# Performance work log

Hardware: AMD Instinct MI355X
Metric: run time of the kernel (lower is better)

## Reference

```python
import jax, jax.numpy as jnp
import numpy as np
from jax import lax

# Module constraint: hidden_dim == state_dim == expand_dim (see broadcasting in original).
H = 128  # hidden_dim
N = 128  # state_dim
E = 128  # expand_dim = hidden_dim * expand_factor (expand_factor=1)
B, L = 4, 1024


def setup_inputs() -> dict:
    key = jax.random.key(0)
    ks = jax.random.split(key, 11)
    s = lambda fan: 1.0 / np.sqrt(fan)
    return {
        "u": jax.random.normal(ks[0], (B, L, H), jnp.float32),
        "W_in": jax.random.normal(ks[1], (H, 2 * E), jnp.float32) * s(H),
        "b_in": jax.random.normal(ks[2], (2 * E,), jnp.float32) * 0.01,
        "conv_w": jax.random.normal(ks[3], (E, 1, 3), jnp.float32) * s(3),
        "conv_b": jax.random.normal(ks[4], (E,), jnp.float32) * 0.01,
        "W_x": jax.random.normal(ks[5], (E, N + N + H), jnp.float32) * s(E),
        "b_x": jax.random.normal(ks[6], (N + N + H,), jnp.float32) * 0.01,
        "A_log": jax.random.normal(ks[7], (N,), jnp.float32),
        "D": jnp.ones((H,), jnp.float32),
        "W_out": jax.random.normal(ks[8], (E, H), jnp.float32) * s(E),
        "b_out": jax.random.normal(ks[9], (H,), jnp.float32) * 0.01,
    }


def reference(u, W_in, b_in, conv_w, conv_b, W_x, b_x, A_log, D, W_out, b_out):
    b, l, _ = u.shape
    xz = u @ W_in + b_in                       # [B,L,2E]
    x, z = jnp.split(xz, 2, axis=-1)           # [B,L,E] each
    # depthwise conv1d, kernel 3, padding 1 (groups == channels)
    xc = lax.conv_general_dilated(
        x.transpose(0, 2, 1), conv_w, window_strides=(1,), padding=[(1, 1)],
        feature_group_count=E, dimension_numbers=("NCH", "OIH", "NCH"))
    x = jax.nn.silu(xc.transpose(0, 2, 1) + conv_b)  # [B,L,E]
    ssm = x @ W_x + b_x                        # [B,L,2N+H]
    delta = jax.nn.softplus(ssm[..., :N])      # [B,L,N]
    Bm = ssm[..., N:2 * N]                     # [B,L,N]
    C = ssm[..., 2 * N:]                       # [B,L,H]
    A = -jnp.exp(A_log)                        # [N]

    def step(h, inp):
        d_t, B_t, C_t, x_t, u_t = inp          # [B,N],[B,N],[B,H],[B,E],[B,H]
        # A_discrete[b,t,i,j] = exp(delta[b,t,i] * A[j])  (outer broadcast, as in source)
        A_disc = jnp.exp(d_t[:, :, None] * A[None, None, :])       # [B,N,N]
        h = A_disc * h + (d_t * B_t)[:, :, None] * x_t[:, None, :]  # [B,N,E]
        y = (h * C_t[:, None, :]).sum(axis=1) + D * u_t             # [B,H]
        return h, y

    h0 = jnp.zeros((b, N, H), u.dtype)
    inputs = (delta.transpose(1, 0, 2), Bm.transpose(1, 0, 2),
              C.transpose(1, 0, 2), x.transpose(1, 0, 2), u.transpose(1, 0, 2))
    _, ys = lax.scan(step, h0, inputs)         # ys: [L,B,H]
    y = ys.transpose(1, 0, 2) * jax.nn.silu(z)  # [B,L,H] (E==H)
    return y @ W_out + b_out                   # dropout in eval mode: identity
```

## Files before the change

### kernel.cpp

```cpp
#include <hip/hip_runtime.h>
#include <hip/hip_bf16.h>

using bf16 = __hip_bfloat16;
typedef __attribute__((ext_vector_type(8))) short short8;
typedef __attribute__((ext_vector_type(4))) float f32x4;

#define BVAL 4
#define LVAL 1024
#define LOG2E 1.44269504f

#define PTS 68

#define OFF_BIN    0
#define OFF_CONVW  256
#define OFF_CONVB  640
#define OFF_BX     768
#define OFF_ALOG   1152
#define OFF_D      1280
#define OFF_BOUT   1408
#define CVT_SMALL  1536

#define R_UBF   524288
#define R_WTIN  (R_UBF + 32768)
#define R_WTX   (R_WTIN + 49152)
#define R_WTOUT (R_WTX + 16384)
#define R_TOT   (R_WTOUT + CVT_SMALL)

__device__ __forceinline__ int dtype_flag(const void* D) {
    return ((*(const unsigned int*)D) & 0xFFFFu) != 0u ? 1 : 0;
}
__device__ __forceinline__ float ldin(const void* p, size_t i, int f) {
    return f ? __bfloat162float(((const bf16*)p)[i]) : ((const float*)p)[i];
}
__device__ __forceinline__ short f2bf(float x) {
    union { bf16 h; short s; } u; u.h = __float2bfloat16(x); return u.s;
}

__global__ void k0_cvt(const void* __restrict__ u, const void* __restrict__ W_in,
                       const void* __restrict__ b_in, const void* __restrict__ conv_w,
                       const void* __restrict__ conv_b, const void* __restrict__ W_x,
                       const void* __restrict__ b_x, const void* __restrict__ A_log,
                       const void* __restrict__ D, const void* __restrict__ W_out,
                       const void* __restrict__ b_out,
                       float* __restrict__ cvt, bf16* __restrict__ ubf,
                       bf16* __restrict__ wtin, bf16* __restrict__ wtx,
                       bf16* __restrict__ wtout) {
    int idx = blockIdx.x * 256 + threadIdx.x;
    if (idx >= R_TOT) return;
    int f = dtype_flag(D);
    if (idx < R_UBF) {
        ubf[idx] = __float2bfloat16(ldin(u, idx, f));
    } else if (idx < R_WTIN) {
        int rel = idx - R_UBF; int n = rel >> 7, k = rel & 127;
        wtin[rel] = __float2bfloat16(ldin(W_in, (size_t)k * 256 + n, f));
    } else if (idx < R_WTX) {
        int rel = idx - R_WTIN; int n = rel >> 7, k = rel & 127;
        wtx[rel] = __float2bfloat16(ldin(W_x, (size_t)k * 384 + n, f));
    } else if (idx < R_WTOUT) {
        int rel = idx - R_WTX; int n = rel >> 7, k = rel & 127;
        wtout[rel] = __float2bfloat16(ldin(W_out, (size_t)k * 128 + n, f));
    } else {
        int rel = idx - R_WTOUT; const void* p; int loc;
        if      (rel < 256)  { p = b_in;   loc = rel; }
        else if (rel < 640)  { p = conv_w; loc = rel - 256; }
        else if (rel < 768)  { p = conv_b; loc = rel - 640; }
        else if (rel < 1152) { p = b_x;    loc = rel - 768; }
        else if (rel < 1280) { p = A_log;  loc = rel - 1152; }
        else if (rel < 1408) { p = D;      loc = rel - 1280; }
        else                 { p = b_out;  loc = rel - 1408; }
        cvt[rel] = ldin(p, loc, f);
    }
}

__global__ void k1_mfma(const bf16* __restrict__ ubf, const bf16* __restrict__ wtin,
                        const float* __restrict__ cvt,
                        float* __restrict__ x_pre, float* __restrict__ zs) {
    int blk = blockIdx.x, mb = blk >> 3, cb = blk & 7;
    int tid = threadIdx.x, w = tid >> 6, lane = tid & 63;
    int quad = lane >> 4, sub = lane & 15;
    int m0 = mb * 64 + w * 16, c = cb * 16;
    f32x4 accX = {0.f, 0.f, 0.f, 0.f}, accZ = {0.f, 0.f, 0.f, 0.f};
    #pragma unroll
    for (int ks = 0; ks < 4; ++ks) {
        int k0 = ks * 32 + quad * 8;
        short8 a  = *(const short8*)(ubf + (size_t)(m0 + sub) * 128 + k0);
        short8 bX = *(const short8*)(wtin + (size_t)(c + sub) * 128 + k0);
        short8 bZ = *(const short8*)(wtin + (size_t)(128 + c + sub) * 128 + k0);
        accX = __builtin_amdgcn_mfma_f32_16x16x32_bf16(a, bX, accX, 0, 0, 0);
        accZ = __builtin_amdgcn_mfma_f32_16x16x32_bf16(a, bZ, accZ, 0, 0, 0);
    }
    int o = c + sub;
    float bx_ = cvt[OFF_BIN + o], bz_ = cvt[OFF_BIN + 128 + o];
    #pragma unroll
    for (int r = 0; r < 4; ++r) {
        int m = m0 + quad * 4 + r;
        float x = accX[r] + bx_;
        float z = accZ[r] + bz_;
        x_pre[(size_t)m * 128 + o] = x;
        zs[(size_t)m * 128 + o] = z / (1.0f + __expf(-z));
    }
}

__global__ void k3_mfma(const float* __restrict__ x_pre, const bf16* __restrict__ wtx,
                        const float* __restrict__ cvt, float* __restrict__ xT,
                        float* __restrict__ dT, float* __restrict__ wT,
                        float* __restrict__ CcT) {
    __shared__ float swc[128 * 4];
    int blk = blockIdx.x, mb = blk >> 3, cb = blk & 7;
    int tid = threadIdx.x, w = tid >> 6, lane = tid & 63;
    int quad = lane >> 4, sub = lane & 15;
    if (tid < 128) {
        swc[tid * 4 + 0] = cvt[OFF_CONVW + tid * 3 + 0];
        swc[tid * 4 + 1] = cvt[OFF_CONVW + tid * 3 + 1];
        swc[tid * 4 + 2] = cvt[OFF_CONVW + tid * 3 + 2];
        swc[tid * 4 + 3] = cvt[OFF_CONVB + tid];
    }
    __syncthreads();
    int m0 = mb * 64 + w * 16, c = cb * 16;
    int row = m0 + sub;
    int l = row & (LVAL - 1);
    const float* xr = x_pre + (size_t)row * 128;
    f32x4 accA = {0.f,0.f,0.f,0.f}, accB = {0.f,0.f,0.f,0.f}, accC = {0.f,0.f,0.f,0.f};
    #pragma unroll
    for (int ks = 0; ks < 4; ++ks) {
        int k0 = ks * 32 + quad * 8;
        float ccv[8], mmv[8], ppv[8];
        *(float4*)&ccv[0] = *(const float4*)(xr + k0);
        *(float4*)&ccv[4] = *(const float4*)(xr + k0 + 4);
        if (l > 0) {
            *(float4*)&mmv[0] = *(const float4*)(xr + k0 - 128);
            *(float4*)&mmv[4] = *(const float4*)(xr + k0 - 124);
        } else {
            #pragma unroll
            for (int i = 0; i < 8; ++i) mmv[i] = 0.f;
        }
        if (l < LVAL - 1) {
            *(float4*)&ppv[0] = *(const float4*)(xr + k0 + 128);
            *(float4*)&ppv[4] = *(const float4*)(xr + k0 + 132);
        } else {
            #pragma unroll
            for (int i = 0; i < 8; ++i) ppv[i] = 0.f;
        }
        float o_[8];
        short8 a;
        #pragma unroll
        for (int i = 0; i < 8; ++i) {
            const float* wc = &swc[(k0 + i) * 4];
            float v = fmaf(wc[0], mmv[i], fmaf(wc[1], ccv[i], fmaf(wc[2], ppv[i], wc[3])));
            o_[i] = v / (1.0f + __expf(-v));
            a[i] = f2bf(o_[i]);
        }
        if (cb == 0) {
            #pragma unroll
            for (int i = 0; i < 8; ++i)
                xT[(size_t)(k0 + i) * 4096 + row] = o_[i];
        }
        short8 bA = *(const short8*)(wtx + (size_t)(c + sub) * 128 + k0);
        short8 bB = *(const short8*)(wtx + (size_t)(128 + c + sub) * 128 + k0);
        short8 bC = *(const short8*)(wtx + (size_t)(256 + c + sub) * 128 + k0);
        accA = __builtin_amdgcn_mfma_f32_16x16x32_bf16(a, bA, accA, 0, 0, 0);
        accB = __builtin_amdgcn_mfma_f32_16x16x32_bf16(a, bB, accB, 0, 0, 0);
        accC = __builtin_amdgcn_mfma_f32_16x16x32_bf16(a, bC, accC, 0, 0, 0);
    }
    int o = c + sub;
    float ba = cvt[OFF_BX + o], bb = cvt[OFF_BX + 128 + o], bc = cvt[OFF_BX + 256 + o];
    float4 spv, dbv, ccv4;
    #pragma unroll
    for (int r = 0; r < 4; ++r) {
        float d = accA[r] + ba;
        float sp = (d > 20.0f) ? d : log1pf(__expf(d));
        ((float*)&spv)[r]  = sp;
        ((float*)&dbv)[r]  = sp * (accB[r] + bb);
        ((float*)&ccv4)[r] = accC[r] + bc;
    }
    int m4 = (m0 >> 2) + quad;
    *(float4*)(dT  + (size_t)m4 * 512 + o * 4)            = spv;
    *(float4*)(wT  + (size_t)m4 * 512 + o * 4)            = dbv;
    *(float4*)(CcT + (size_t)o * 4096 + m0 + quad * 4)    = ccv4;
}

__global__ __launch_bounds__(256, 1)
void k5_scan(const float* __restrict__ cvt, const float* __restrict__ dT,
             const float* __restrict__ wT, const float* __restrict__ xT,
             const float* __restrict__ CcT, float* __restrict__ pP0) {
    __shared__ float pt[4][32][PTS];
    const size_t NEc = (size_t)BVAL * LVAL * 128;
    int blk = blockIdx.x;
    int half = blk & 1, jq = (blk >> 1) & 31, b = blk >> 6;
    int tid = threadIdx.x, w = tid >> 6, lane = tid & 63;
    int j = jq * 4 + w;
    size_t base = (size_t)b * LVAL * 128;
    float* __restrict__ pP = pP0 + (size_t)half * NEc;
    float a2 = -__expf(cvt[OFF_ALOG + j]) * LOG2E;
    const float4* gd4 = (const float4*)dT + (size_t)b * 256 * 128 + half * 64 + lane;
    const float4* gw4 = (const float4*)wT + (size_t)b * 256 * 128 + half * 64 + lane;
    const float4* gx4 = (const float4*)(xT + (size_t)j * 4096 + b * 1024);
    const float*  gcp = CcT + (size_t)j * 4096 + b * 1024;
    float (*ptw)[PTS] = pt[w];
    int rr = lane >> 2, rq = lane & 3;
    float h = 0.f;

#define LOADC(dq, wq, xq, c0v, c1v, cc) { \
    _Pragma("unroll") \
    for (int q = 0; q < 8; ++q) { \
        dq[q] = gd4[((cc) * 8 + q) * 128]; \
        wq[q] = gw4[((cc) * 8 + q) * 128]; \
        xq[q] = gx4[(cc) * 8 + q]; \
    } \
    c0v = gcp[(cc) * 32 + rr]; \
    c1v = gcp[(cc) * 32 + 16 + rr]; }

#define STEP(dv, wv, xv, row) { \
    float e_ = exp2f((dv) * a2); \
    h = fmaf(e_, h, (wv) * (xv)); \
    ptw[row][lane] = h; }

#define QSTEP(dq, wq, xq, q) \
    STEP(dq[q].x, wq[q].x, xq[q].x, (q) * 4 + 0) \
    STEP(dq[q].y, wq[q].y, xq[q].y, (q) * 4 + 1) \
    STEP(dq[q].z, wq[q].z, xq[q].z, (q) * 4 + 2) \
    STEP(dq[q].w, wq[q].w, xq[q].w, (q) * 4 + 3)

#define REDUCE(g, ccv, cc) { \
    const float4* pr_ = (const float4*)&ptw[(g) * 16 + rr][rq * 16]; \
    float4 v0_ = pr_[0], v1_ = pr_[1], v2_ = pr_[2], v3_ = pr_[3]; \
    float s_ = ((v0_.x + v0_.y) + (v0_.z + v0_.w)) + ((v1_.x + v1_.y) + (v1_.z + v1_.w)) \
             + ((v2_.x + v2_.y) + (v2_.z + v2_.w)) + ((v3_.x + v3_.y) + (v3_.z + v3_.w)); \
    s_ += __shfl_xor(s_, 1, 64); \
    s_ += __shfl_xor(s_, 2, 64); \
    if (rq == 0) { \
        int t_ = (cc) * 32 + (g) * 16 + rr; \
        pP[base + (size_t)t_ * 128 + j] = (ccv) * s_; } }

#define COMPUTE(dq, wq, xq, c0v, c1v, cc) { \
    QSTEP(dq, wq, xq, 0) QSTEP(dq, wq, xq, 1) QSTEP(dq, wq, xq, 2) QSTEP(dq, wq, xq, 3) \
    QSTEP(dq, wq, xq, 4) QSTEP(dq, wq, xq, 5) QSTEP(dq, wq, xq, 6) QSTEP(dq, wq, xq, 7) \
    __builtin_amdgcn_wave_barrier(); \
    REDUCE(0, c0v, cc) \
    REDUCE(1, c1v, cc) \
    __builtin_amdgcn_wave_barrier(); }

    float4 dqA[8], wqA[8], xqA[8], dqB[8], wqB[8], xqB[8];
    float cA0, cA1, cB0, cB1;
    LOADC(dqA, wqA, xqA, cA0, cA1, 0);
    for (int c = 0; c < 32; c += 2) {
        LOADC(dqB, wqB, xqB, cB0, cB1, c + 1);
        COMPUTE(dqA, wqA, xqA, cA0, cA1, c);
        if (c + 2 < 32) LOADC(dqA, wqA, xqA, cA0, cA1, c + 2);
        COMPUTE(dqB, wqB, xqB, cB0, cB1, c + 1);
    }
#undef LOADC
#undef STEP
#undef QSTEP
#undef REDUCE
#undef COMPUTE
}

__global__ void k6_mfma(const float* __restrict__ pA, const float* __restrict__ pB,
                        const float* __restrict__ zs, const void* __restrict__ uin,
                        const bf16* __restrict__ wtout, const float* __restrict__ cvt,
                        const void* __restrict__ Din, void* __restrict__ out) {
    int blk = blockIdx.x, mb = blk >> 2, nb = blk & 3;
    int tid = threadIdx.x, w = tid >> 6, lane = tid & 63;
    int quad = lane >> 4, sub = lane & 15;
    int m0 = mb * 64 + w * 16, n0 = nb * 32;
    int f = dtype_flag(Din);
    int row = m0 + sub;
    f32x4 acc0 = {0.f,0.f,0.f,0.f}, acc1 = {0.f,0.f,0.f,0.f};
    #pragma unroll
    for (int ks = 0; ks < 4; ++ks) {
        int k0 = ks * 32 + quad * 8;
        size_t ri = (size_t)row * 128 + k0;
        float av[8], bv[8], zv[8], dv[8];
        *(float4*)&av[0] = *(const float4*)(pA + ri);
        *(float4*)&av[4] = *(const float4*)(pA + ri + 4);
        *(float4*)&bv[0] = *(const float4*)(pB + ri);
        *(float4*)&bv[4] = *(const float4*)(pB + ri + 4);
        *(float4*)&zv[0] = *(const float4*)(zs + ri);
        *(float4*)&zv[4] = *(const float4*)(zs + ri + 4);
        *(float4*)&dv[0] = *(const float4*)(cvt + OFF_D + k0);
        *(float4*)&dv[4] = *(const float4*)(cvt + OFF_D + k0 + 4);
        short8 a;
        #pragma unroll
        for (int i = 0; i < 8; ++i) {
            float uu = ldin(uin, ri + i, f);
            float v = (av[i] + bv[i] + dv[i] * uu) * zv[i];
            a[i] = f2bf(v);
        }
        short8 b0 = *(const short8*)(wtout + (size_t)(n0 + sub) * 128 + k0);
        short8 b1 = *(const short8*)(wtout + (size_t)(n0 + 16 + sub) * 128 + k0);
        acc0 = __builtin_amdgcn_mfma_f32_16x16x32_bf16(a, b0, acc0, 0, 0, 0);
        acc1 = __builtin_amdgcn_mfma_f32_16x16x32_bf16(a, b1, acc1, 0, 0, 0);
    }
    float bo0 = cvt[OFF_BOUT + n0 + sub], bo1 = cvt[OFF_BOUT + n0 + 16 + sub];
    #pragma unroll
    for (int r = 0; r < 4; ++r) {
        int m = m0 + quad * 4 + r;
        float v0 = acc0[r] + bo0, v1 = acc1[r] + bo1;
        if (f) {
            ((bf16*)out)[(size_t)m * 128 + n0 + sub] = __float2bfloat16(v0);
            ((bf16*)out)[(size_t)m * 128 + n0 + 16 + sub] = __float2bfloat16(v1);
        } else {
            ((float*)out)[(size_t)m * 128 + n0 + sub] = v0;
            ((float*)out)[(size_t)m * 128 + n0 + 16 + sub] = v1;
        }
    }
}

extern "C" void kernel_launch(void* const* d_in, const int* in_sizes, int n_in,
                              void* d_out, int out_size, void* d_ws, size_t ws_size,
                              hipStream_t stream) {
    const size_t NE = (size_t)BVAL * LVAL * 128;

    float* cvt   = (float*)d_ws;
    float* bufs  = cvt + 2048;
    float* x_pre = bufs + 0 * NE;
    float* zs    = bufs + 1 * NE;
    float* xT    = bufs + 2 * NE;
    float* dT    = bufs + 3 * NE;
    float* wT    = bufs + 4 * NE;
    float* CcT   = bufs + 5 * NE;
    float* pA    = bufs + 6 * NE;
    bf16* ubf    = (bf16*)(bufs + 8 * NE);
    bf16* wtin   = ubf + NE;
    bf16* wtx    = wtin + 32768;
    bf16* wtout  = wtx + 49152;

    k0_cvt<<<(R_TOT + 255) / 256, 256, 0, stream>>>(
        d_in[0], d_in[1], d_in[2], d_in[3], d_in[4], d_in[5],
        d_in[6], d_in[7], d_in[8], d_in[9], d_in[10],
        cvt, ubf, wtin, wtx, wtout);
    k1_mfma<<<512, 256, 0, stream>>>(ubf, wtin, cvt, x_pre, zs);
    k3_mfma<<<512, 256, 0, stream>>>(x_pre, wtx, cvt, xT, dT, wT, CcT);
    k5_scan<<<256, 256, 0, stream>>>(cvt, dT, wT, xT, CcT, pA);
    k6_mfma<<<256, 256, 0, stream>>>(pA, pA + NE, zs, d_in[0], wtout, cvt,
                                     d_in[8], d_out);
}
```

Measured before the change: 155.4 us.

## Split sequential scan into chunked three-pass parallel scan over eight segments

Replaces the single sequential scan kernel, which launched 256 blocks each walking 1024 timesteps, with a three-phase chunked scan. Phase one computes per-segment final states and cumulative decay products over 128-step segments. A small combine kernel propagates carries across the 8 segments, and phase two reruns each segment from its seed while doing the C-weighted reduction. This exposes 8x more blocks to fill the GPU, at the cost of reading the inputs twice and two extra launches.

```diff
diff --git a/kernel.cpp b/kernel.cpp
--- a/kernel.cpp
+++ b/kernel.cpp
@@ -179,81 +179,95 @@
     *(float4*)(CcT + (size_t)o * 4096 + m0 + quad * 4)    = ccv4;
 }
 
-__global__ __launch_bounds__(256, 1)
-void k5_scan(const float* __restrict__ cvt, const float* __restrict__ dT,
-             const float* __restrict__ wT, const float* __restrict__ xT,
-             const float* __restrict__ CcT, float* __restrict__ pP0) {
-    __shared__ float pt[4][32][PTS];
+
+__global__ __launch_bounds__(256, 8)
+void k5a_scan(const float* __restrict__ cvt, const float* __restrict__ dT,
+              const float* __restrict__ wT, const float* __restrict__ xT,
+              float* __restrict__ hfin, float* __restrict__ Pfin) {
+    int blk = blockIdx.x;
+    int seg = blk & 7, half = (blk >> 3) & 1, jq = (blk >> 4) & 31, b = blk >> 9;
+    int tid = threadIdx.x, w = tid >> 6, lane = tid & 63;
+    int j = jq * 4 + w, ni = half * 64 + lane;
+    int t0 = b * 1024 + seg * 128;
+    float a2 = -__expf(cvt[OFF_ALOG + j]) * LOG2E;
+    const float4* gd4 = (const float4*)dT + (size_t)(t0 >> 2) * 128 + ni;
+    const float4* gw4 = (const float4*)wT + (size_t)(t0 >> 2) * 128 + ni;
+    const float4* gx4 = (const float4*)(xT + (size_t)j * 4096 + t0);
+    float h = 0.f, sd = 0.f;
+#define P1S(dv, wv, xv) { h = fmaf(exp2f((dv) * a2), h, (wv) * (xv)); sd += (dv); }
+    for (int c = 0; c < 16; ++c) {
+        float4 d0 = gd4[(c * 2 + 0) * 128], d1 = gd4[(c * 2 + 1) * 128];
+        float4 w0 = gw4[(c * 2 + 0) * 128], w1 = gw4[(c * 2 + 1) * 128];
+        float4 x0 = gx4[c * 2 + 0],         x1 = gx4[c * 2 + 1];
+        P1S(d0.x, w0.x, x0.x) P1S(d0.y, w0.y, x0.y)
+        P1S(d0.z, w0.z, x0.z) P1S(d0.w, w0.w, x0.w)
+        P1S(d1.x, w1.x, x1.x) P1S(d1.y, w1.y, x1.y)
+        P1S(d1.z, w1.z, x1.z) P1S(d1.w, w1.w, x1.w)
+    }
+#undef P1S
+    size_t fi = ((size_t)(seg * 4 + b) * 128 + j) * 128 + ni;
+    hfin[fi] = h;
+    Pfin[fi] = exp2f(sd * a2);
+}
+
+__global__ void k5b_comb(const float* __restrict__ hfin, const float* __restrict__ Pfin,
+                         float* __restrict__ seeds) {
+    int q = blockIdx.x * 256 + threadIdx.x;
+    int n = q & 127, j = (q >> 7) & 127, b = q >> 14;
+    float s = 0.f;
+    #pragma unroll
+    for (int seg = 0; seg < 8; ++seg) {
+        size_t idx = ((size_t)(seg * 4 + b) * 128 + j) * 128 + n;
+        seeds[idx] = s;
+        s = fmaf(Pfin[idx], s, hfin[idx]);
+    }
+}
+
+__global__ __launch_bounds__(256, 8)
+void k5c_scan(const float* __restrict__ cvt, const float* __restrict__ dT,
+              const float* __restrict__ wT, const float* __restrict__ xT,
+              const float* __restrict__ CcT, const float* __restrict__ seeds,
+              float* __restrict__ pP0) {
+    __shared__ float pt[4][8][PTS];
     const size_t NEc = (size_t)BVAL * LVAL * 128;
     int blk = blockIdx.x;
-    int half = blk & 1, jq = (blk >> 1) & 31, b = blk >> 6;
-    int tid = threadIdx.x, w = tid >> 6, lane = tid & 63;
-    int j = jq * 4 + w;
+    int seg = blk & 7, half = (blk >> 3) & 1, jq = (blk >> 4) & 31, b = blk >> 9;
+    int tid = threadIdx.x, w = tid >> 6, lane = tid & 63;
+    int j = jq * 4 + w, ni = half * 64 + lane;
+    int t0 = b * 1024 + seg * 128;
     size_t base = (size_t)b * LVAL * 128;
     float* __restrict__ pP = pP0 + (size_t)half * NEc;
     float a2 = -__expf(cvt[OFF_ALOG + j]) * LOG2E;
-    const float4* gd4 = (const float4*)dT + (size_t)b * 256 * 128 + half * 64 + lane;
-    const float4* gw4 = (const float4*)wT + (size_t)b * 256 * 128 + half * 64 + lane;
-    const float4* gx4 = (const float4*)(xT + (size_t)j * 4096 + b * 1024);
-    const float*  gcp = CcT + (size_t)j * 4096 + b * 1024;
+    const float4* gd4 = (const float4*)dT + (size_t)(t0 >> 2) * 128 + ni;
+    const float4* gw4 = (const float4*)wT + (size_t)(t0 >> 2) * 128 + ni;
+    const float4* gx4 = (const float4*)(xT + (size_t)j * 4096 + t0);
+    const float*  gcp = CcT + (size_t)j * 4096 + t0;
     float (*ptw)[PTS] = pt[w];
-    int rr = lane >> 2, rq = lane & 3;
-    float h = 0.f;
-
-#define LOADC(dq, wq, xq, c0v, c1v, cc) { \
-    _Pragma("unroll") \
-    for (int q = 0; q < 8; ++q) { \
-        dq[q] = gd4[((cc) * 8 + q) * 128]; \
-        wq[q] = gw4[((cc) * 8 + q) * 128]; \
-        xq[q] = gx4[(cc) * 8 + q]; \
-    } \
-    c0v = gcp[(cc) * 32 + rr]; \
-    c1v = gcp[(cc) * 32 + 16 + rr]; }
-
-#define STEP(dv, wv, xv, row) { \
-    float e_ = exp2f((dv) * a2); \
-    h = fmaf(e_, h, (wv) * (xv)); \
-    ptw[row][lane] = h; }
-
-#define QSTEP(dq, wq, xq, q) \
-    STEP(dq[q].x, wq[q].x, xq[q].x, (q) * 4 + 0) \
-    STEP(dq[q].y, wq[q].y, xq[q].y, (q) * 4 + 1) \
-    STEP(dq[q].z, wq[q].z, xq[q].z, (q) * 4 + 2) \
-    STEP(dq[q].w, wq[q].w, xq[q].w, (q) * 4 + 3)
-
-#define REDUCE(g, ccv, cc) { \
-    const float4* pr_ = (const float4*)&ptw[(g) * 16 + rr][rq * 16]; \
-    float4 v0_ = pr_[0], v1_ = pr_[1], v2_ = pr_[2], v3_ = pr_[3]; \
-    float s_ = ((v0_.x + v0_.y) + (v0_.z + v0_.w)) + ((v1_.x + v1_.y) + (v1_.z + v1_.w)) \
-             + ((v2_.x + v2_.y) + (v2_.z + v2_.w)) + ((v3_.x + v3_.y) + (v3_.z + v3_.w)); \
-    s_ += __shfl_xor(s_, 1, 64); \
-    s_ += __shfl_xor(s_, 2, 64); \
-    if (rq == 0) { \
-        int t_ = (cc) * 32 + (g) * 16 + rr; \
-        pP[base + (size_t)t_ * 128 + j] = (ccv) * s_; } }
-
-#define COMPUTE(dq, wq, xq, c0v, c1v, cc) { \
-    QSTEP(dq, wq, xq, 0) QSTEP(dq, wq, xq, 1) QSTEP(dq, wq, xq, 2) QSTEP(dq, wq, xq, 3) \
-    QSTEP(dq, wq, xq, 4) QSTEP(dq, wq, xq, 5) QSTEP(dq, wq, xq, 6) QSTEP(dq, wq, xq, 7) \
-    __builtin_amdgcn_wave_barrier(); \
-    REDUCE(0, c0v, cc) \
-    REDUCE(1, c1v, cc) \
-    __builtin_amdgcn_wave_barrier(); }
-
-    float4 dqA[8], wqA[8], xqA[8], dqB[8], wqB[8], xqB[8];
-    float cA0, cA1, cB0, cB1;
-    LOADC(dqA, wqA, xqA, cA0, cA1, 0);
-    for (int c = 0; c < 32; c += 2) {
-        LOADC(dqB, wqB, xqB, cB0, cB1, c + 1);
-        COMPUTE(dqA, wqA, xqA, cA0, cA1, c);
-        if (c + 2 < 32) LOADC(dqA, wqA, xqA, cA0, cA1, c + 2);
-        COMPUTE(dqB, wqB, xqB, cB0, cB1, c + 1);
-    }
-#undef LOADC
-#undef STEP
-#undef QSTEP
-#undef REDUCE
-#undef COMPUTE
+    int rr = lane >> 3, rq = lane & 7;
+    float h = seeds[((size_t)(seg * 4 + b) * 128 + j) * 128 + ni];
+#define P2S(dv, wv, xv, row) { h = fmaf(exp2f((dv) * a2), h, (wv) * (xv)); \
+                               ptw[row][lane] = h; }
+    for (int c = 0; c < 16; ++c) {
+        float4 d0 = gd4[(c * 2 + 0) * 128], d1 = gd4[(c * 2 + 1) * 128];
+        float4 w0 = gw4[(c * 2 + 0) * 128], w1 = gw4[(c * 2 + 1) * 128];
+        float4 x0 = gx4[c * 2 + 0],         x1 = gx4[c * 2 + 1];
+        float cv = gcp[c * 8 + rr];
+        P2S(d0.x, w0.x, x0.x, 0) P2S(d0.y, w0.y, x0.y, 1)
+        P2S(d0.z, w0.z, x0.z, 2) P2S(d0.w, w0.w, x0.w, 3)
+        P2S(d1.x, w1.x, x1.x, 4) P2S(d1.y, w1.y, x1.y, 5)
+        P2S(d1.z, w1.z, x1.z, 6) P2S(d1.w, w1.w, x1.w, 7)
+        const float4* pr = (const float4*)&ptw[rr][rq * 8];
+        float4 v0 = pr[0], v1 = pr[1];
+        float s = ((v0.x + v0.y) + (v0.z + v0.w)) + ((v1.x + v1.y) + (v1.z + v1.w));
+        s += __shfl_xor(s, 1, 64);
+        s += __shfl_xor(s, 2, 64);
+        s += __shfl_xor(s, 4, 64);
+        if (rq == 0) {
+            int tl = seg * 128 + c * 8 + rr;
+            pP[base + (size_t)tl * 128 + j] = cv * s;
+        }
+    }
+#undef P2S
 }
 
 __global__ void k6_mfma(const float* __restrict__ pA, const float* __restrict__ pB,
@@ -321,7 +335,10 @@
     float* wT    = bufs + 4 * NE;
     float* CcT   = bufs + 5 * NE;
     float* pA    = bufs + 6 * NE;
-    bf16* ubf    = (bf16*)(bufs + 8 * NE);
+    float* hfin  = bufs + 8 * NE;
+    float* Pfin  = bufs + 9 * NE;
+    float* seeds = bufs + 10 * NE;
+    bf16* ubf    = (bf16*)(bufs + 11 * NE);
     bf16* wtin   = ubf + NE;
     bf16* wtx    = wtin + 32768;
     bf16* wtout  = wtx + 49152;
@@ -332,7 +349,9 @@
         cvt, ubf, wtin, wtx, wtout);
     k1_mfma<<<512, 256, 0, stream>>>(ubf, wtin, cvt, x_pre, zs);
     k3_mfma<<<512, 256, 0, stream>>>(x_pre, wtx, cvt, xT, dT, wT, CcT);
-    k5_scan<<<256, 256, 0, stream>>>(cvt, dT, wT, xT, CcT, pA);
+    k5a_scan<<<2048, 256, 0, stream>>>(cvt, dT, wT, xT, hfin, Pfin);
+    k5b_comb<<<256, 256, 0, stream>>>(hfin, Pfin, seeds);
+    k5c_scan<<<2048, 256, 0, stream>>>(cvt, dT, wT, xT, CcT, seeds, pA);
     k6_mfma<<<256, 256, 0, stream>>>(pA, pA + NE, zs, d_in[0], wtout, cvt,
                                      d_in[8], d_out);
 }
```

Result: slower. 162.2 us (+4.3%).
